# Kernel optimization log

Hardware: AMD Instinct MI355X
Metric: run time of the kernel (lower is better)

## Reference

```python
import jax, jax.numpy as jnp
import numpy as np


def _conv3x3(x, w, b):
    # x: [B,C,H,W], w: [O,C,3,3], b: [O]; stride 1, padding 1 (SAME)
    y = jax.lax.conv_general_dilated(
        x, w, window_strides=(1, 1), padding='SAME',
        dimension_numbers=('NCHW', 'OIHW', 'NCHW'))
    return y + b[None, :, None, None]


def setup_inputs() -> dict:
    key = jax.random.key(0)
    ks = jax.random.split(key, 7)
    B, C, H, W = 8, 256, 48, 48
    emb = 512
    fan_out = emb * 9  # kaiming_normal_ fan_out, relu gain sqrt(2)
    std = float(np.sqrt(2.0 / fan_out))
    feat = jax.random.normal(ks[0], (B, C, H, W), dtype=jnp.float32)
    Wq = jax.random.normal(ks[1], (emb, C, 3, 3), dtype=jnp.float32) * std
    Wk = jax.random.normal(ks[2], (emb, C, 3, 3), dtype=jnp.float32) * std
    Wv = jax.random.normal(ks[3], (emb, C, 3, 3), dtype=jnp.float32) * std
    bound = 1.0 / np.sqrt(C * 9)
    bq = jax.random.uniform(ks[4], (emb,), jnp.float32, -bound, bound)
    bk = jax.random.uniform(ks[5], (emb,), jnp.float32, -bound, bound)
    bv = jax.random.uniform(ks[6], (emb,), jnp.float32, -bound, bound)
    return {"feat": feat, "Wq": Wq, "bq": bq, "Wk": Wk, "bk": bk, "Wv": Wv, "bv": bv}


def reference(feat, Wq, bq, Wk, bk, Wv, bv):
    B, C, H, W = feat.shape
    emb = Wq.shape[0]
    q = _conv3x3(feat, Wq, bq).reshape(B, emb, H * W)  # [B,E,N]
    k = _conv3x3(feat, Wk, bk).reshape(B, emb, H * W)
    v = _conv3x3(feat, Wv, bv).reshape(B, emb, H * W)
    # att[b,i,j] = <q[:, i], k[:, j]>, softmax over j (keys)
    att = jnp.einsum('bei,bej->bij', q, k)
    att = jax.nn.softmax(att, axis=2)
    # v_att[b,e,i] = sum_j v[b,e,j] * att[b,i,j]
    v_att = jnp.einsum('bej,bij->bei', v, att)
    return v_att.reshape(B, emb, H, W) + v.reshape(B, emb, H, W)
```

## Files before the change

kernel.cpp:

```cpp
#include <hip/hip_runtime.h>


typedef _Float16 f16;
typedef _Float16 f16x4 __attribute__((ext_vector_type(4)));
typedef _Float16 f16x8 __attribute__((ext_vector_type(8)));
typedef float    f32x4  __attribute__((ext_vector_type(4)));
typedef float    f32x16 __attribute__((ext_vector_type(16)));

__device__ __forceinline__ f32x16 mfma16(f16x8 a, f16x8 b, f32x16 c) {
  return __builtin_amdgcn_mfma_f32_32x32x16_f16(a, b, c, 0, 0, 0);
}

__device__ __forceinline__ f16x8 f16x8_zero() {
  f16x8 z;
#pragma unroll
  for (int j = 0; j < 8; ++j) z[j] = (f16)0.f;
  return z;
}

#define NB   8
#define NC   256
#define NH   48
#define NN   2304
#define NE   512
#define HP   50


__global__ void pack_feat(const float* __restrict__ x, f16* __restrict__ p) {
  __shared__ f16 tx[48 * 258];
  const int b = blockIdx.x, yp = blockIdx.y;
  const int tid = threadIdx.x;
  f16* prow = p + ((size_t)(b * HP + yp) * HP) * NC;

  if (yp == 0 || yp == HP - 1) {
    for (int i = tid; i < 1600; i += 256)
      *(f16x8*)(prow + i * 8) = f16x8_zero();
    return;
  }
  const int y = yp - 1;
#pragma unroll 4
  for (int it = 0; it < 64; ++it) {
    int i = it * 256 + tid;
    int xsl = i & 63, c = i >> 6;
    if (xsl < 48) {
      float v = x[((b * NC + c) * NH + y) * NH + xsl];
      tx[xsl * 258 + c] = (f16)v;
    }
  }
  __syncthreads();
#pragma unroll
  for (int it = 0; it < 6; ++it) {
    int xq = (tid >> 5) + it * 8;
    int c0 = (tid & 31) * 8;
    f16x8 v = *(const f16x8*)(tx + xq * 258 + c0);
    *(f16x8*)(prow + (xq + 1) * NC + c0) = v;
  }
  if (tid < 64) {
    int xp = (tid >> 5) * (HP - 1);
    int c0 = (tid & 31) * 8;
    *(f16x8*)(prow + xp * NC + c0) = f16x8_zero();
  }
}

__global__ void pack_w(const float* __restrict__ wq, const float* __restrict__ wk,
                       const float* __restrict__ wv,
                       f16* __restrict__ oq, f16* __restrict__ ok,
                       f16* __restrict__ ov) {
  int idx = blockIdx.x * 256 + threadIdx.x;
  int c = idx & 255;
  int r = idx >> 8;
  int e = r & 511; int t = r >> 9;
  int src = (e * NC + c) * 9 + t;
  int cc = c >> 4, cl = c & 15, et = e >> 5, el = e & 31;
  int dst = ((cc * 9 + t) * 16 + et) * 512 + el * 16 + cl;
  oq[dst] = (f16)wq[src];
  ok[dst] = (f16)wk[src];
  ov[dst] = (f16)wv[src];
}

__global__ __launch_bounds__(256, 3) void conv3_all(
    const f16* __restrict__ xh,
    const f16* __restrict__ wq, const f16* __restrict__ wk,
    const f16* __restrict__ wv,
    const float* __restrict__ bq, const float* __restrict__ bk,
    const float* __restrict__ bv,
    f16* __restrict__ oq, f16* __restrict__ okf, f16* __restrict__ ovf) {
  __shared__ __align__(16) f16 sx[2][12000];

  const int tid = threadIdx.x;
  const int lane = tid & 63, wvx = tid >> 6;
  const int l31 = lane & 31;
  const int koff = (lane >> 5) * 8;
  const int et = blockIdx.x;
  const int e0 = et * 32;
  const int by = blockIdx.y;
  const int b = by / 6, strip = by % 6;
  const int y0 = strip * 8;
  const int F = blockIdx.z;
  const f16* w = (F == 0) ? wq : (F == 1) ? wk : wv;
  const float* bias = (F == 0) ? bq : (F == 1) ? bk : bv;

  int pb[3];
#pragma unroll
  for (int nt = 0; nt < 3; ++nt) {
    int n = wvx * 96 + nt * 32 + l31;
    pb[nt] = (n / 48) * 50 + (n % 48);
  }

  int sgp[4], sgo[4]; bool sok[4]; int gbase[4];
#pragma unroll
  for (int u = 0; u < 4; ++u) {
    int g = u * 256 + tid;
    sok[u] = (g < 1000);
    int gg = sok[u] ? g : 999;
    sgp[u] = gg >> 1; sgo[u] = (gg & 1) * 8;
    int row = sgp[u] / 50, xx = sgp[u] % 50;
    gbase[u] = ((b * HP + y0 + row) * HP + xx) * NC + sgo[u];
  }

  f32x16 acc[3];
#pragma unroll
  for (int nt = 0; nt < 3; ++nt)
#pragma unroll
    for (int i = 0; i < 16; ++i) acc[nt][i] = 0.f;

  const int wlocal = l31 * 16 + koff;

  {
    f16x8 rx0[4];
#pragma unroll
    for (int u = 0; u < 4; ++u)
      rx0[u] = *(const f16x8*)(xh + gbase[u]);
#pragma unroll
    for (int u = 0; u < 4; ++u)
      if (sok[u]) *(f16x8*)(sx[0] + sgp[u] * 24 + sgo[u]) = rx0[u];
  }
  __syncthreads();

  for (int cc = 0; cc < 16; ++cc) {
    f16x8 wreg[9];
#pragma unroll
    for (int t = 0; t < 9; ++t)
      wreg[t] = *(const f16x8*)(w + ((cc * 9 + t) * 16 + et) * 512 + wlocal);
    f16x8 rx[4];
    if (cc < 15) {
      int c0 = (cc + 1) * 16;
#pragma unroll
      for (int u = 0; u < 4; ++u)
        rx[u] = *(const f16x8*)(xh + gbase[u] + c0);
    }
    const f16* sxc = sx[cc & 1];
#pragma unroll
    for (int t = 0; t < 9; ++t) {
      const int dy = t / 3, dx = t % 3;
      const int dpo = (dy * 50 + dx) * 24 + koff;
#pragma unroll
      for (int nt = 0; nt < 3; ++nt) {
        f16x8 bh = *(const f16x8*)(sxc + pb[nt] * 24 + dpo);
        acc[nt] = mfma16(wreg[t], bh, acc[nt]);
      }
    }
    if (cc < 15) {
#pragma unroll
      for (int u = 0; u < 4; ++u)
        if (sok[u]) *(f16x8*)(sx[(cc + 1) & 1] + sgp[u] * 24 + sgo[u]) = rx[u];
    }
    __syncthreads();
  }

  const int colh = (lane >> 5) * 4;
#pragma unroll
  for (int nt = 0; nt < 3; ++nt) {
    int n = wvx * 96 + nt * 32 + l31;
    int pos = (y0 + n / 48) * 48 + (n % 48);
    const int jblk = pos >> 5, jl = pos & 31;
    const int jc = pos >> 4, lhv = (pos >> 3) & 1, uv = pos & 7;
#pragma unroll
    for (int g = 0; g < 4; ++g) {
      int eb = e0 + g * 8 + colh;
      f32x4 sb = *(const f32x4*)(bias + eb);
      if (F == 0) {
        f16x4 hq;
#pragma unroll
        for (int j = 0; j < 4; ++j) hq[j] = (f16)(acc[nt][g * 4 + j] + sb[j]);
        *(f16x4*)(oq + ((size_t)b * NN + pos) * NE + eb) = hq;
      } else if (F == 1) {
        f16x4 hk;
#pragma unroll
        for (int j = 0; j < 4; ++j) hk[j] = (f16)(acc[nt][g * 4 + j] + sb[j]);
        *(f16x4*)(okf + ((((size_t)b * 72 + jblk) * 32 + (eb >> 4)) * 64 +
                         ((eb >> 3) & 1) * 32 + jl) * 8 + (eb & 7)) = hk;
      } else {
#pragma unroll
        for (int j = 0; j < 4; ++j) {
          int e = eb + j;
          ovf[((((size_t)b * 16 + (e >> 5)) * 144 + jc) * 64 + lhv * 32 + (e & 31)) * 8 + uv] =
              (f16)(acc[nt][g * 4 + j] + sb[j]);
        }
      }
    }
  }
}

__global__ __launch_bounds__(256, 2) void attn(
    const f16* __restrict__ qt, const f16* __restrict__ kf,
    const f16* __restrict__ vf, float* __restrict__ out) {
  __shared__ __align__(16) f16 q_lds[16384];
  __shared__ __align__(16) f16 sP2[4096];
  __shared__ __align__(16) float s_pmax[128];
  __shared__ __align__(16) float s_psum[128];

  const int tid = threadIdx.x;
  const int lane = tid & 63, wvx = tid >> 6;
  const int l31 = lane & 31, lh = lane >> 5;
  const int bid = blockIdx.x;
  const int b = bid & 7;
  const int i0 = (bid >> 3) * 32;

  const f16* kfw = kf + (size_t)(b * 72 + wvx) * 16384 + lane * 8;
  const f16* vfw = vf + (size_t)(b * 16 + wvx * 4) * 73728 + lane * 8;

  {
    const f16* qb = qt + ((size_t)b * NN + i0) * NE;
#pragma unroll
    for (int it = 0; it < 8; ++it) {
      int g = it * 256 + tid;
      int row = g >> 6, gr = g & 63;
      f16x8 v = *(const f16x8*)(qb + row * NE + gr * 8);
      *(f16x8*)(q_lds + (gr >> 1) * 512 + (gr & 1) * 256 + row * 8) = v;
    }
  }
  f16x8 kpipe[12];
#pragma unroll
  for (int t = 0; t < 12; ++t) kpipe[t] = *(const f16x8*)(kfw + t * 512);
  __syncthreads();

  float m_reg = -1e30f, l_reg = 0.f;
  f32x16 O[4];
#pragma unroll
  for (int nt = 0; nt < 4; ++nt)
#pragma unroll
    for (int i = 0; i < 16; ++i) O[nt][i] = 0.f;

  const f16* qlw = q_lds + lane * 8;
  f16x8 vpipe[12];

  for (int jt = 0; jt < 18; ++jt) {
    const f16* kfl = kfw + (size_t)jt * 4 * 16384;
    const f16* vfl = vfw + (size_t)jt * 8 * 512;

    f32x16 S0, S1;
#pragma unroll
    for (int i = 0; i < 16; ++i) { S0[i] = 0.f; S1[i] = 0.f; }
#pragma unroll
    for (int c = 0; c < 32; ++c) {
      f16x8 ak = kpipe[c % 12];
      if (c + 12 < 32) kpipe[c % 12] = *(const f16x8*)(kfl + (c + 12) * 512);
      f16x8 aq = *(const f16x8*)(qlw + c * 512);
      if (c & 1) S1 = mfma16(ak, aq, S1);
      else       S0 = mfma16(ak, aq, S0);
    }
#pragma unroll
    for (int t = 0; t < 12; ++t) {
      int nt = t & 3, cg = t >> 2;
      vpipe[t] = *(const f16x8*)(vfl + (size_t)nt * 73728 + cg * 512);
    }
    f32x16 S;
#pragma unroll
    for (int r = 0; r < 16; ++r) S[r] = S0[r] + S1[r];

    float wmax = S[0];
#pragma unroll
    for (int r = 1; r < 16; ++r) wmax = fmaxf(wmax, S[r]);
    wmax = fmaxf(wmax, __shfl_xor(wmax, 32, 64));
    if (lane < 32) s_pmax[l31 * 4 + wvx] = wmax;
    __syncthreads();
    f32x4 pm4 = *(const f32x4*)(s_pmax + l31 * 4);
    float gmax = fmaxf(fmaxf(pm4[0], pm4[1]), fmaxf(pm4[2], pm4[3]));
    float mnew = fmaxf(m_reg, gmax);
    float alpha = __expf(m_reg - mnew);
    m_reg = mnew;

    f16 ph[16];
    float psum = 0.f;
#pragma unroll
    for (int r = 0; r < 16; ++r) {
      f16 p = (f16)__expf(S[r] - mnew);
      ph[r] = p;
      psum += (float)p;
    }
    union Q4 { f16x4 h; int i2[2]; };
    Q4 q4[4];
#pragma unroll
    for (int t = 0; t < 4; ++t)
#pragma unroll
      for (int u = 0; u < 4; ++u) q4[t].h[u] = ph[t * 4 + u];
#pragma unroll
    for (int ks = 0; ks < 2; ++ks) {
      Q4 t1, t2;
      t1.i2[0] = __shfl_xor(q4[2 * ks + 1].i2[0], 32, 64);
      t1.i2[1] = __shfl_xor(q4[2 * ks + 1].i2[1], 32, 64);
      t2.i2[0] = __shfl_xor(q4[2 * ks].i2[0], 32, 64);
      t2.i2[1] = __shfl_xor(q4[2 * ks].i2[1], 32, 64);
      f16x4 first  = lh ? t1.h : q4[2 * ks].h;
      f16x4 second = lh ? q4[2 * ks + 1].h : t2.h;
      f16x8 frag;
#pragma unroll
      for (int u = 0; u < 4; ++u) { frag[u] = first[u]; frag[4 + u] = second[u]; }
      *(f16x8*)(sP2 + ((wvx * 2 + ks) * 64 + lane) * 8) = frag;
    }
    psum += __shfl_xor(psum, 32, 64);
    if (lane < 32) s_psum[l31 * 4 + wvx] = psum;
#pragma unroll
    for (int nt = 0; nt < 4; ++nt)
#pragma unroll
      for (int r = 0; r < 16; ++r) O[nt][r] *= alpha;
    __syncthreads();
    f32x4 ps4 = *(const f32x4*)(s_psum + l31 * 4);
    l_reg = l_reg * alpha + (ps4[0] + ps4[1] + ps4[2] + ps4[3]);

    if (jt < 17) {
      const f16* kn = kfw + (size_t)(jt + 1) * 4 * 16384;
#pragma unroll
      for (int t = 0; t < 12; ++t) kpipe[t] = *(const f16x8*)(kn + t * 512);
    }
    f16x8 apc = *(const f16x8*)(sP2 + (0 * 64 + lane) * 8);
    f16x8 apn = *(const f16x8*)(sP2 + (1 * 64 + lane) * 8);
#pragma unroll
    for (int c = 0; c < 32; ++c) {
      int nt = c & 3, cg = c >> 2;
      f16x8 av = vpipe[c % 12];
      if (c + 12 < 32) {
        int c2 = c + 12, nt2 = c2 & 3, cg2 = c2 >> 2;
        vpipe[c % 12] = *(const f16x8*)(vfl + (size_t)nt2 * 73728 + cg2 * 512);
      }
      O[nt] = mfma16(av, apc, O[nt]);
      if (nt == 3) {
        apc = apn;
        if (cg + 2 < 8) apn = *(const f16x8*)(sP2 + ((cg + 2) * 64 + lane) * 8);
      }
    }
  }

  float inv = 1.0f / l_reg;
  const int ii = i0 + l31;
  const int jcR = ii >> 4, lhR = (ii >> 3) & 1, uR = ii & 7;
#pragma unroll
  for (int nt = 0; nt < 4; ++nt) {
    const f16* vres = vf + ((((size_t)(b * 16 + wvx * 4 + nt)) * 144 + jcR) * 64 + lhR * 32) * 8 + uR;
    const int ebase = wvx * 128 + nt * 32;
#pragma unroll
    for (int r = 0; r < 16; ++r) {
      int el = (r & 3) + 8 * (r >> 2) + 4 * lh;
      float rv = (float)vres[el * 8];
      out[((size_t)b * NE + ebase + el) * NN + ii] = O[nt][r] * inv + rv;
    }
  }
}

extern "C" void kernel_launch(void* const* d_in, const int* in_sizes, int n_in,
                              void* d_out, int out_size, void* d_ws, size_t ws_size,
                              hipStream_t stream) {
  const float* feat = (const float*)d_in[0];
  const float* Wq = (const float*)d_in[1];
  const float* bq = (const float*)d_in[2];
  const float* Wk = (const float*)d_in[3];
  const float* bk = (const float*)d_in[4];
  const float* Wv = (const float*)d_in[5];
  const float* bv = (const float*)d_in[6];
  float* out = (float*)d_out;

  char* ws = (char*)d_ws;
  size_t off = 0;
  auto alloc = [&](size_t bytes) {
    void* p = ws + off;
    off += (bytes + 255) & ~(size_t)255;
    return p;
  };
  const size_t FP = (size_t)NB * HP * HP * NC;
  const size_t WP = (size_t)9 * NE * NC;
  const size_t QP = (size_t)NB * NN * NE;
  f16* fp  = (f16*)alloc(FP * 2);
  f16* wq  = (f16*)alloc(WP * 2);
  f16* wk  = (f16*)alloc(WP * 2);
  f16* wv  = (f16*)alloc(WP * 2);
  f16* q_t = (f16*)alloc(QP * 2);
  f16* k_f = (f16*)alloc(QP * 2);
  f16* v_f = (f16*)alloc(QP * 2);

  pack_feat<<<dim3(NB, HP), dim3(256), 0, stream>>>(feat, fp);
  pack_w<<<dim3(WP / 256), dim3(256), 0, stream>>>(Wq, Wk, Wv, wq, wk, wv);

  conv3_all<<<dim3(16, 48, 3), dim3(256), 0, stream>>>(
      fp, wq, wk, wv, bq, bk, bv, q_t, k_f, v_f);

  attn<<<dim3(576), dim3(256), 0, stream>>>(q_t, k_f, v_f, out);
}
```

Baseline: 434.9 us.

## Split attention over key halves with combine kernel; stage conv weights in LDS

```diff
diff --git a/kernel.cpp b/kernel.cpp
--- a/kernel.cpp
+++ b/kernel.cpp
@@ -85,18 +85,20 @@
     const float* __restrict__ bq, const float* __restrict__ bk,
     const float* __restrict__ bv,
     f16* __restrict__ oq, f16* __restrict__ okf, f16* __restrict__ ovf) {
-  __shared__ __align__(16) f16 sx[2][12000];
+  __shared__ __align__(16) f16 sx[12000];
+  __shared__ __align__(16) f16 sw[4608];
 
   const int tid = threadIdx.x;
   const int lane = tid & 63, wvx = tid >> 6;
   const int l31 = lane & 31;
   const int koff = (lane >> 5) * 8;
-  const int et = blockIdx.x;
+  const int bid = blockIdx.x;
+  const int b = bid & 7;
+  int r = bid >> 3;
+  const int strip = r % 6; r /= 6;
+  const int et = r & 15, F = r >> 4;
   const int e0 = et * 32;
-  const int by = blockIdx.y;
-  const int b = by / 6, strip = by % 6;
   const int y0 = strip * 8;
-  const int F = blockIdx.z;
   const f16* w = (F == 0) ? wq : (F == 1) ? wk : wv;
   const float* bias = (F == 0) ? bq : (F == 1) ? bk : bv;
 
@@ -117,6 +119,18 @@
     int row = sgp[u] / 50, xx = sgp[u] % 50;
     gbase[u] = ((b * HP + y0 + row) * HP + xx) * NC + sgo[u];
   }
+  int wgt[3], wgj[3], wdst[3]; bool wok[3];
+#pragma unroll
+  for (int u = 0; u < 3; ++u) {
+    int g = u * 256 + tid;
+    wok[u] = (g < 576);
+    int gg = wok[u] ? g : 575;
+    wgt[u] = gg >> 6; wgj[u] = gg & 63;
+    int wjs = wgj[u] ^ ((wgj[u] >> 3) & 7);
+    wdst[u] = wgt[u] * 512 + wjs * 8;
+  }
+  const int j8 = 2 * l31 + (lane >> 5);
+  const int wread = (j8 ^ ((j8 >> 3) & 7)) * 8;
 
   f32x16 acc[3];
 #pragma unroll
@@ -124,48 +138,43 @@
 #pragma unroll
     for (int i = 0; i < 16; ++i) acc[nt][i] = 0.f;
 
-  const int wlocal = l31 * 16 + koff;
-
-  {
-    f16x8 rx0[4];
+  f16x8 rx[4], rw[3];
+#pragma unroll
+  for (int u = 0; u < 4; ++u)
+    rx[u] = *(const f16x8*)(xh + gbase[u]);
+#pragma unroll
+  for (int u = 0; u < 3; ++u)
+    rw[u] = *(const f16x8*)(w + ((0 * 9 + wgt[u]) * 16 + et) * 512 + wgj[u] * 8);
+
+  for (int cc = 0; cc < 16; ++cc) {
+    __syncthreads();
 #pragma unroll
     for (int u = 0; u < 4; ++u)
-      rx0[u] = *(const f16x8*)(xh + gbase[u]);
-#pragma unroll
-    for (int u = 0; u < 4; ++u)
-      if (sok[u]) *(f16x8*)(sx[0] + sgp[u] * 24 + sgo[u]) = rx0[u];
-  }
-  __syncthreads();
-
-  for (int cc = 0; cc < 16; ++cc) {
-    f16x8 wreg[9];
-#pragma unroll
-    for (int t = 0; t < 9; ++t)
-      wreg[t] = *(const f16x8*)(w + ((cc * 9 + t) * 16 + et) * 512 + wlocal);
-    f16x8 rx[4];
+      if (sok[u]) *(f16x8*)(sx + sgp[u] * 24 + sgo[u]) = rx[u];
+#pragma unroll
+    for (int u = 0; u < 3; ++u)
+      if (wok[u]) *(f16x8*)(sw + wdst[u]) = rw[u];
+    __syncthreads();
     if (cc < 15) {
       int c0 = (cc + 1) * 16;
 #pragma unroll
       for (int u = 0; u < 4; ++u)
         rx[u] = *(const f16x8*)(xh + gbase[u] + c0);
-    }
-    const f16* sxc = sx[cc & 1];
+#pragma unroll
+      for (int u = 0; u < 3; ++u)
+        rw[u] = *(const f16x8*)(w + (((cc + 1) * 9 + wgt[u]) * 16 + et) * 512 + wgj[u] * 8);
+    }
 #pragma unroll
     for (int t = 0; t < 9; ++t) {
+      f16x8 aw = *(const f16x8*)(sw + t * 512 + wread);
       const int dy = t / 3, dx = t % 3;
       const int dpo = (dy * 50 + dx) * 24 + koff;
 #pragma unroll
       for (int nt = 0; nt < 3; ++nt) {
-        f16x8 bh = *(const f16x8*)(sxc + pb[nt] * 24 + dpo);
-        acc[nt] = mfma16(wreg[t], bh, acc[nt]);
+        f16x8 bh = *(const f16x8*)(sx + pb[nt] * 24 + dpo);
+        acc[nt] = mfma16(aw, bh, acc[nt]);
       }
     }
-    if (cc < 15) {
-#pragma unroll
-      for (int u = 0; u < 4; ++u)
-        if (sok[u]) *(f16x8*)(sx[(cc + 1) & 1] + sgp[u] * 24 + sgo[u]) = rx[u];
-    }
-    __syncthreads();
   }
 
   const int colh = (lane >> 5) * 4;
@@ -202,9 +211,10 @@
   }
 }
 
-__global__ __launch_bounds__(256, 2) void attn(
+__global__ __launch_bounds__(256, 3) void attn(
     const f16* __restrict__ qt, const f16* __restrict__ kf,
-    const f16* __restrict__ vf, float* __restrict__ out) {
+    const f16* __restrict__ vf, f16* __restrict__ po,
+    float* __restrict__ pm, float* __restrict__ pl) {
   __shared__ __align__(16) f16 q_lds[16384];
   __shared__ __align__(16) f16 sP2[4096];
   __shared__ __align__(16) float s_pmax[128];
@@ -215,10 +225,9 @@
   const int l31 = lane & 31, lh = lane >> 5;
   const int bid = blockIdx.x;
   const int b = bid & 7;
-  const int i0 = (bid >> 3) * 32;
-
-  const f16* kfw = kf + (size_t)(b * 72 + wvx) * 16384 + lane * 8;
-  const f16* vfw = vf + (size_t)(b * 16 + wvx * 4) * 73728 + lane * 8;
+  const int t2 = bid >> 3;
+  const int i0 = (t2 % 72) * 32;
+  const int jh = t2 / 72;
 
   {
     const f16* qb = qt + ((size_t)b * NN + i0) * NE;
@@ -230,9 +239,6 @@
       *(f16x8*)(q_lds + (gr >> 1) * 512 + (gr & 1) * 256 + row * 8) = v;
     }
   }
-  f16x8 kpipe[12];
-#pragma unroll
-  for (int t = 0; t < 12; ++t) kpipe[t] = *(const f16x8*)(kfw + t * 512);
   __syncthreads();
 
   float m_reg = -1e30f, l_reg = 0.f;
@@ -242,28 +248,25 @@
 #pragma unroll
     for (int i = 0; i < 16; ++i) O[nt][i] = 0.f;
 
+  const f16* kfw = kf + (size_t)(b * 72 + jh * 36 + wvx) * 16384 + lane * 8;
+  const f16* vfw = vf + (size_t)(b * 16 + wvx * 4) * 73728 + (size_t)jh * 72 * 512 + lane * 8;
   const f16* qlw = q_lds + lane * 8;
-  f16x8 vpipe[12];
-
-  for (int jt = 0; jt < 18; ++jt) {
+
+  for (int jt = 0; jt < 9; ++jt) {
     const f16* kfl = kfw + (size_t)jt * 4 * 16384;
-    const f16* vfl = vfw + (size_t)jt * 8 * 512;
-
     f32x16 S0, S1;
 #pragma unroll
     for (int i = 0; i < 16; ++i) { S0[i] = 0.f; S1[i] = 0.f; }
+    f16x8 kpipe[6];
+#pragma unroll
+    for (int t = 0; t < 6; ++t) kpipe[t] = *(const f16x8*)(kfl + t * 512);
 #pragma unroll
     for (int c = 0; c < 32; ++c) {
-      f16x8 ak = kpipe[c % 12];
-      if (c + 12 < 32) kpipe[c % 12] = *(const f16x8*)(kfl + (c + 12) * 512);
+      f16x8 ak = kpipe[c % 6];
+      if (c + 6 < 32) kpipe[c % 6] = *(const f16x8*)(kfl + (c + 6) * 512);
       f16x8 aq = *(const f16x8*)(qlw + c * 512);
       if (c & 1) S1 = mfma16(ak, aq, S1);
       else       S0 = mfma16(ak, aq, S0);
-    }
-#pragma unroll
-    for (int t = 0; t < 12; ++t) {
-      int nt = t & 3, cg = t >> 2;
-      vpipe[t] = *(const f16x8*)(vfl + (size_t)nt * 73728 + cg * 512);
     }
     f32x16 S;
 #pragma unroll
@@ -297,13 +300,13 @@
       for (int u = 0; u < 4; ++u) q4[t].h[u] = ph[t * 4 + u];
 #pragma unroll
     for (int ks = 0; ks < 2; ++ks) {
-      Q4 t1, t2;
-      t1.i2[0] = __shfl_xor(q4[2 * ks + 1].i2[0], 32, 64);
-      t1.i2[1] = __shfl_xor(q4[2 * ks + 1].i2[1], 32, 64);
-      t2.i2[0] = __shfl_xor(q4[2 * ks].i2[0], 32, 64);
-      t2.i2[1] = __shfl_xor(q4[2 * ks].i2[1], 32, 64);
-      f16x4 first  = lh ? t1.h : q4[2 * ks].h;
-      f16x4 second = lh ? q4[2 * ks + 1].h : t2.h;
+      Q4 t1a, t2a;
+      t1a.i2[0] = __shfl_xor(q4[2 * ks + 1].i2[0], 32, 64);
+      t1a.i2[1] = __shfl_xor(q4[2 * ks + 1].i2[1], 32, 64);
+      t2a.i2[0] = __shfl_xor(q4[2 * ks].i2[0], 32, 64);
+      t2a.i2[1] = __shfl_xor(q4[2 * ks].i2[1], 32, 64);
+      f16x4 first  = lh ? t1a.h : q4[2 * ks].h;
+      f16x4 second = lh ? q4[2 * ks + 1].h : t2a.h;
       f16x8 frag;
 #pragma unroll
       for (int u = 0; u < 4; ++u) { frag[u] = first[u]; frag[4 + u] = second[u]; }
@@ -319,20 +322,22 @@
     f32x4 ps4 = *(const f32x4*)(s_psum + l31 * 4);
     l_reg = l_reg * alpha + (ps4[0] + ps4[1] + ps4[2] + ps4[3]);
 
-    if (jt < 17) {
-      const f16* kn = kfw + (size_t)(jt + 1) * 4 * 16384;
-#pragma unroll
-      for (int t = 0; t < 12; ++t) kpipe[t] = *(const f16x8*)(kn + t * 512);
+    const f16* vfl = vfw + (size_t)jt * 8 * 512;
+    f16x8 vpipe[6];
+#pragma unroll
+    for (int t = 0; t < 6; ++t) {
+      int nt = t & 3, cg = t >> 2;
+      vpipe[t] = *(const f16x8*)(vfl + (size_t)nt * 73728 + cg * 512);
     }
     f16x8 apc = *(const f16x8*)(sP2 + (0 * 64 + lane) * 8);
     f16x8 apn = *(const f16x8*)(sP2 + (1 * 64 + lane) * 8);
 #pragma unroll
     for (int c = 0; c < 32; ++c) {
       int nt = c & 3, cg = c >> 2;
-      f16x8 av = vpipe[c % 12];
-      if (c + 12 < 32) {
-        int c2 = c + 12, nt2 = c2 & 3, cg2 = c2 >> 2;
-        vpipe[c % 12] = *(const f16x8*)(vfl + (size_t)nt2 * 73728 + cg2 * 512);
+      f16x8 av = vpipe[c % 6];
+      if (c + 6 < 32) {
+        int nt2 = (c + 6) & 3, cg2 = (c + 6) >> 2;
+        vpipe[c % 6] = *(const f16x8*)(vfl + (size_t)nt2 * 73728 + cg2 * 512);
       }
       O[nt] = mfma16(av, apc, O[nt]);
       if (nt == 3) {
@@ -342,20 +347,50 @@
     }
   }
 
-  float inv = 1.0f / l_reg;
+  if (tid < 32) {
+    pm[(jh * NB + b) * NN + i0 + tid] = m_reg;
+    pl[(jh * NB + b) * NN + i0 + tid] = l_reg;
+  }
+  const size_t pobase = ((size_t)(jh * NB + b) * NE) * NN;
   const int ii = i0 + l31;
-  const int jcR = ii >> 4, lhR = (ii >> 3) & 1, uR = ii & 7;
 #pragma unroll
   for (int nt = 0; nt < 4; ++nt) {
-    const f16* vres = vf + ((((size_t)(b * 16 + wvx * 4 + nt)) * 144 + jcR) * 64 + lhR * 32) * 8 + uR;
     const int ebase = wvx * 128 + nt * 32;
 #pragma unroll
     for (int r = 0; r < 16; ++r) {
       int el = (r & 3) + 8 * (r >> 2) + 4 * lh;
-      float rv = (float)vres[el * 8];
-      out[((size_t)b * NE + ebase + el) * NN + ii] = O[nt][r] * inv + rv;
-    }
-  }
+      po[pobase + (size_t)(ebase + el) * NN + ii] = (f16)O[nt][r];
+    }
+  }
+}
+
+__global__ void combine(const f16* __restrict__ po, const float* __restrict__ pm,
+                        const float* __restrict__ pl, const f16* __restrict__ vf,
+                        float* __restrict__ out) {
+  int id = blockIdx.x * 256 + threadIdx.x;
+  int base = id * 4;
+  int i  = base % NN;
+  int eb = base / NN;
+  int b  = eb >> 9;
+  int e  = eb & 511;
+  const size_t H = (size_t)NB * NE * NN;
+  f32x4 m0 = *(const f32x4*)(pm + b * NN + i);
+  f32x4 m1 = *(const f32x4*)(pm + NB * NN + b * NN + i);
+  f32x4 l0 = *(const f32x4*)(pl + b * NN + i);
+  f32x4 l1 = *(const f32x4*)(pl + NB * NN + b * NN + i);
+  f16x4 a0 = *(const f16x4*)(po + (size_t)eb * NN + i);
+  f16x4 a1 = *(const f16x4*)(po + H + (size_t)eb * NN + i);
+  f16x4 vv = *(const f16x4*)(vf + ((((size_t)(b * 16 + (e >> 5))) * 144 + (i >> 4)) * 64 +
+                                   ((i >> 3) & 1) * 32 + (e & 31)) * 8 + (i & 7));
+  f32x4 res;
+#pragma unroll
+  for (int j = 0; j < 4; ++j) {
+    float m = fmaxf(m0[j], m1[j]);
+    float w0 = __expf(m0[j] - m), w1 = __expf(m1[j] - m);
+    float l = w0 * l0[j] + w1 * l1[j];
+    res[j] = (w0 * (float)a0[j] + w1 * (float)a1[j]) / l + (float)vv[j];
+  }
+  *(f32x4*)(out + (size_t)eb * NN + i) = res;
 }
 
 extern "C" void kernel_launch(void* const* d_in, const int* in_sizes, int n_in,
@@ -387,12 +422,16 @@
   f16* q_t = (f16*)alloc(QP * 2);
   f16* k_f = (f16*)alloc(QP * 2);
   f16* v_f = (f16*)alloc(QP * 2);
+  f16* po  = (f16*)alloc(2 * QP * 2);
+  float* pm = (float*)alloc(2 * (size_t)NB * NN * 4);
+  float* pl = (float*)alloc(2 * (size_t)NB * NN * 4);
 
   pack_feat<<<dim3(NB, HP), dim3(256), 0, stream>>>(feat, fp);
   pack_w<<<dim3(WP / 256), dim3(256), 0, stream>>>(Wq, Wk, Wv, wq, wk, wv);
 
-  conv3_all<<<dim3(16, 48, 3), dim3(256), 0, stream>>>(
+  conv3_all<<<dim3(2304), dim3(256), 0, stream>>>(
       fp, wq, wk, wv, bq, bk, bv, q_t, k_f, v_f);
 
-  attn<<<dim3(576), dim3(256), 0, stream>>>(q_t, k_f, v_f, out);
-}
+  attn<<<dim3(1152), dim3(256), 0, stream>>>(q_t, k_f, v_f, po, pm, pl);
+  combine<<<dim3((NB * NE * NN / 4) / 256), dim3(256), 0, stream>>>(po, pm, pl, v_f, out);
+}
```

Result: slower. 447.4 us (+2.9%).

## Stage conv weights in swizzled LDS, remap grid, shrink attention register pipelines

Applied to the files above, without the earlier changes.

```diff
diff --git a/kernel.cpp b/kernel.cpp
--- a/kernel.cpp
+++ b/kernel.cpp
@@ -85,18 +85,20 @@
     const float* __restrict__ bq, const float* __restrict__ bk,
     const float* __restrict__ bv,
     f16* __restrict__ oq, f16* __restrict__ okf, f16* __restrict__ ovf) {
-  __shared__ __align__(16) f16 sx[2][12000];
+  __shared__ __align__(16) f16 sx[12000];
+  __shared__ __align__(16) f16 sw[4608];
 
   const int tid = threadIdx.x;
   const int lane = tid & 63, wvx = tid >> 6;
   const int l31 = lane & 31;
   const int koff = (lane >> 5) * 8;
-  const int et = blockIdx.x;
+  const int bid = blockIdx.x;
+  const int b = bid & 7;
+  int r = bid >> 3;
+  const int strip = r % 6; r /= 6;
+  const int et = r & 15, F = r >> 4;
   const int e0 = et * 32;
-  const int by = blockIdx.y;
-  const int b = by / 6, strip = by % 6;
   const int y0 = strip * 8;
-  const int F = blockIdx.z;
   const f16* w = (F == 0) ? wq : (F == 1) ? wk : wv;
   const float* bias = (F == 0) ? bq : (F == 1) ? bk : bv;
 
@@ -117,6 +119,18 @@
     int row = sgp[u] / 50, xx = sgp[u] % 50;
     gbase[u] = ((b * HP + y0 + row) * HP + xx) * NC + sgo[u];
   }
+  int wgt[3], wgj[3], wdst[3]; bool wok[3];
+#pragma unroll
+  for (int u = 0; u < 3; ++u) {
+    int g = u * 256 + tid;
+    wok[u] = (g < 576);
+    int gg = wok[u] ? g : 575;
+    wgt[u] = gg >> 6; wgj[u] = gg & 63;
+    int wjs = wgj[u] ^ ((wgj[u] >> 3) & 7);
+    wdst[u] = wgt[u] * 512 + wjs * 8;
+  }
+  const int j8 = 2 * l31 + (lane >> 5);
+  const int wread = (j8 ^ ((j8 >> 3) & 7)) * 8;
 
   f32x16 acc[3];
 #pragma unroll
@@ -124,48 +138,43 @@
 #pragma unroll
     for (int i = 0; i < 16; ++i) acc[nt][i] = 0.f;
 
-  const int wlocal = l31 * 16 + koff;
-
-  {
-    f16x8 rx0[4];
+  f16x8 rx[4], rw[3];
+#pragma unroll
+  for (int u = 0; u < 4; ++u)
+    rx[u] = *(const f16x8*)(xh + gbase[u]);
+#pragma unroll
+  for (int u = 0; u < 3; ++u)
+    rw[u] = *(const f16x8*)(w + ((0 * 9 + wgt[u]) * 16 + et) * 512 + wgj[u] * 8);
+
+  for (int cc = 0; cc < 16; ++cc) {
+    __syncthreads();
 #pragma unroll
     for (int u = 0; u < 4; ++u)
-      rx0[u] = *(const f16x8*)(xh + gbase[u]);
-#pragma unroll
-    for (int u = 0; u < 4; ++u)
-      if (sok[u]) *(f16x8*)(sx[0] + sgp[u] * 24 + sgo[u]) = rx0[u];
-  }
-  __syncthreads();
-
-  for (int cc = 0; cc < 16; ++cc) {
-    f16x8 wreg[9];
-#pragma unroll
-    for (int t = 0; t < 9; ++t)
-      wreg[t] = *(const f16x8*)(w + ((cc * 9 + t) * 16 + et) * 512 + wlocal);
-    f16x8 rx[4];
+      if (sok[u]) *(f16x8*)(sx + sgp[u] * 24 + sgo[u]) = rx[u];
+#pragma unroll
+    for (int u = 0; u < 3; ++u)
+      if (wok[u]) *(f16x8*)(sw + wdst[u]) = rw[u];
+    __syncthreads();
     if (cc < 15) {
       int c0 = (cc + 1) * 16;
 #pragma unroll
       for (int u = 0; u < 4; ++u)
         rx[u] = *(const f16x8*)(xh + gbase[u] + c0);
-    }
-    const f16* sxc = sx[cc & 1];
+#pragma unroll
+      for (int u = 0; u < 3; ++u)
+        rw[u] = *(const f16x8*)(w + (((cc + 1) * 9 + wgt[u]) * 16 + et) * 512 + wgj[u] * 8);
+    }
 #pragma unroll
     for (int t = 0; t < 9; ++t) {
+      f16x8 aw = *(const f16x8*)(sw + t * 512 + wread);
       const int dy = t / 3, dx = t % 3;
       const int dpo = (dy * 50 + dx) * 24 + koff;
 #pragma unroll
       for (int nt = 0; nt < 3; ++nt) {
-        f16x8 bh = *(const f16x8*)(sxc + pb[nt] * 24 + dpo);
-        acc[nt] = mfma16(wreg[t], bh, acc[nt]);
+        f16x8 bh = *(const f16x8*)(sx + pb[nt] * 24 + dpo);
+        acc[nt] = mfma16(aw, bh, acc[nt]);
       }
     }
-    if (cc < 15) {
-#pragma unroll
-      for (int u = 0; u < 4; ++u)
-        if (sok[u]) *(f16x8*)(sx[(cc + 1) & 1] + sgp[u] * 24 + sgo[u]) = rx[u];
-    }
-    __syncthreads();
   }
 
   const int colh = (lane >> 5) * 4;
@@ -202,7 +211,7 @@
   }
 }
 
-__global__ __launch_bounds__(256, 2) void attn(
+__global__ __launch_bounds__(256, 3) void attn(
     const f16* __restrict__ qt, const f16* __restrict__ kf,
     const f16* __restrict__ vf, float* __restrict__ out) {
   __shared__ __align__(16) f16 q_lds[16384];
@@ -217,9 +226,6 @@
   const int b = bid & 7;
   const int i0 = (bid >> 3) * 32;
 
-  const f16* kfw = kf + (size_t)(b * 72 + wvx) * 16384 + lane * 8;
-  const f16* vfw = vf + (size_t)(b * 16 + wvx * 4) * 73728 + lane * 8;
-
   {
     const f16* qb = qt + ((size_t)b * NN + i0) * NE;
 #pragma unroll
@@ -230,9 +236,6 @@
       *(f16x8*)(q_lds + (gr >> 1) * 512 + (gr & 1) * 256 + row * 8) = v;
     }
   }
-  f16x8 kpipe[12];
-#pragma unroll
-  for (int t = 0; t < 12; ++t) kpipe[t] = *(const f16x8*)(kfw + t * 512);
   __syncthreads();
 
   float m_reg = -1e30f, l_reg = 0.f;
@@ -242,32 +245,25 @@
 #pragma unroll
     for (int i = 0; i < 16; ++i) O[nt][i] = 0.f;
 
+  const f16* kfw = kf + (size_t)(b * 72 + wvx) * 16384 + lane * 8;
+  const f16* vfw = vf + (size_t)(b * 16 + wvx * 4) * 73728 + lane * 8;
   const f16* qlw = q_lds + lane * 8;
-  f16x8 vpipe[12];
 
   for (int jt = 0; jt < 18; ++jt) {
     const f16* kfl = kfw + (size_t)jt * 4 * 16384;
-    const f16* vfl = vfw + (size_t)jt * 8 * 512;
-
-    f32x16 S0, S1;
-#pragma unroll
-    for (int i = 0; i < 16; ++i) { S0[i] = 0.f; S1[i] = 0.f; }
+    f32x16 S;
+#pragma unroll
+    for (int i = 0; i < 16; ++i) S[i] = 0.f;
+    f16x8 kpipe[8];
+#pragma unroll
+    for (int t = 0; t < 8; ++t) kpipe[t] = *(const f16x8*)(kfl + t * 512);
 #pragma unroll
     for (int c = 0; c < 32; ++c) {
-      f16x8 ak = kpipe[c % 12];
-      if (c + 12 < 32) kpipe[c % 12] = *(const f16x8*)(kfl + (c + 12) * 512);
+      f16x8 ak = kpipe[c & 7];
+      if (c + 8 < 32) kpipe[c & 7] = *(const f16x8*)(kfl + (c + 8) * 512);
       f16x8 aq = *(const f16x8*)(qlw + c * 512);
-      if (c & 1) S1 = mfma16(ak, aq, S1);
-      else       S0 = mfma16(ak, aq, S0);
-    }
-#pragma unroll
-    for (int t = 0; t < 12; ++t) {
-      int nt = t & 3, cg = t >> 2;
-      vpipe[t] = *(const f16x8*)(vfl + (size_t)nt * 73728 + cg * 512);
-    }
-    f32x16 S;
-#pragma unroll
-    for (int r = 0; r < 16; ++r) S[r] = S0[r] + S1[r];
+      S = mfma16(ak, aq, S);
+    }
 
     float wmax = S[0];
 #pragma unroll
@@ -278,14 +274,21 @@
     f32x4 pm4 = *(const f32x4*)(s_pmax + l31 * 4);
     float gmax = fmaxf(fmaxf(pm4[0], pm4[1]), fmaxf(pm4[2], pm4[3]));
     float mnew = fmaxf(m_reg, gmax);
-    float alpha = __expf(m_reg - mnew);
-    m_reg = mnew;
+    float alpha = 1.f;
+    if (!__all(mnew == m_reg)) {
+      alpha = __expf(m_reg - mnew);
+      m_reg = mnew;
+#pragma unroll
+      for (int nt = 0; nt < 4; ++nt)
+#pragma unroll
+        for (int r = 0; r < 16; ++r) O[nt][r] *= alpha;
+    }
 
     f16 ph[16];
     float psum = 0.f;
 #pragma unroll
     for (int r = 0; r < 16; ++r) {
-      f16 p = (f16)__expf(S[r] - mnew);
+      f16 p = (f16)__expf(S[r] - m_reg);
       ph[r] = p;
       psum += (float)p;
     }
@@ -311,28 +314,26 @@
     }
     psum += __shfl_xor(psum, 32, 64);
     if (lane < 32) s_psum[l31 * 4 + wvx] = psum;
-#pragma unroll
-    for (int nt = 0; nt < 4; ++nt)
-#pragma unroll
-      for (int r = 0; r < 16; ++r) O[nt][r] *= alpha;
     __syncthreads();
     f32x4 ps4 = *(const f32x4*)(s_psum + l31 * 4);
     l_reg = l_reg * alpha + (ps4[0] + ps4[1] + ps4[2] + ps4[3]);
 
-    if (jt < 17) {
-      const f16* kn = kfw + (size_t)(jt + 1) * 4 * 16384;
-#pragma unroll
-      for (int t = 0; t < 12; ++t) kpipe[t] = *(const f16x8*)(kn + t * 512);
+    const f16* vfl = vfw + (size_t)jt * 8 * 512;
+    f16x8 vpipe[8];
+#pragma unroll
+    for (int t = 0; t < 8; ++t) {
+      int nt = t & 3, cg = t >> 2;
+      vpipe[t] = *(const f16x8*)(vfl + (size_t)nt * 73728 + cg * 512);
     }
     f16x8 apc = *(const f16x8*)(sP2 + (0 * 64 + lane) * 8);
     f16x8 apn = *(const f16x8*)(sP2 + (1 * 64 + lane) * 8);
 #pragma unroll
     for (int c = 0; c < 32; ++c) {
       int nt = c & 3, cg = c >> 2;
-      f16x8 av = vpipe[c % 12];
-      if (c + 12 < 32) {
-        int c2 = c + 12, nt2 = c2 & 3, cg2 = c2 >> 2;
-        vpipe[c % 12] = *(const f16x8*)(vfl + (size_t)nt2 * 73728 + cg2 * 512);
+      f16x8 av = vpipe[c & 7];
+      if (c + 8 < 32) {
+        int c2 = c + 8, nt2 = c2 & 3, cg2 = c2 >> 2;
+        vpipe[c & 7] = *(const f16x8*)(vfl + (size_t)nt2 * 73728 + cg2 * 512);
       }
       O[nt] = mfma16(av, apc, O[nt]);
       if (nt == 3) {
@@ -391,7 +392,7 @@
   pack_feat<<<dim3(NB, HP), dim3(256), 0, stream>>>(feat, fp);
   pack_w<<<dim3(WP / 256), dim3(256), 0, stream>>>(Wq, Wk, Wv, wq, wk, wv);
 
-  conv3_all<<<dim3(16, 48, 3), dim3(256), 0, stream>>>(
+  conv3_all<<<dim3(2304), dim3(256), 0, stream>>>(
       fp, wq, wk, wv, bq, bk, bv, q_t, k_f, v_f);
 
   attn<<<dim3(576), dim3(256), 0, stream>>>(q_t, k_f, v_f, out);
```

Result: faster. 381.6 us (-12.3%).
